# Kernel tuning notes

Hardware: AMD Instinct MI355X
Metric: run time of the kernel (lower is better)

Reference implementation:

```python
import jax, jax.numpy as jnp
import numpy as np

NUM_TEAMS = 200000
EMBED_DIM = 16
NUM_EDGES = 3200000
BATCH = 500000
EPS_NORM = 1e-12  # F.normalize clamp
EPS_SOFTMAX = 1e-16  # PyG edge-softmax denom eps
NEG_SLOPE = 0.01  # LeakyReLU default


def setup_inputs() -> dict:
    key = jax.random.key(0)
    ks = jax.random.split(key, 12)
    inp = {}
    inp["embed"] = jax.random.normal(ks[0], (NUM_TEAMS, EMBED_DIM), dtype=jnp.float32)
    inp["beta"] = jnp.ones((2,), dtype=jnp.float32)  # one learnable scalar per AGNNConv
    # torch Linear init ~ U(-1/sqrt(fan_in), 1/sqrt(fan_in)); stored as [in, out]
    def lin(k, fi, fo):
        b = 1.0 / np.sqrt(fi)
        k1, k2 = jax.random.split(k)
        return (jax.random.uniform(k1, (fi, fo), jnp.float32, -b, b),
                jax.random.uniform(k2, (fo,), jnp.float32, -b, b))
    inp["lin0_w"], inp["lin0_b"] = lin(ks[1], 2 * EMBED_DIM, 6)
    inp["lin1_w"], inp["lin1_b"] = lin(ks[2], 6, 16)
    inp["lin2_w"], inp["lin2_b"] = lin(ks[3], 16, 3)
    inp["edge_index"] = jax.random.randint(ks[4], (2, NUM_EDGES), 0, NUM_TEAMS, dtype=jnp.int64)
    inp["home"] = jax.random.randint(ks[5], (BATCH,), 0, NUM_TEAMS, dtype=jnp.int64)
    inp["away"] = jax.random.randint(ks[6], (BATCH,), 0, NUM_TEAMS, dtype=jnp.int64)
    return inp


def _agnn_conv(x, beta, src, dst, n):
    # x: [N, D]; messages flow src(j) -> dst(i); scatter-softmax over edges per dst
    xn = x / jnp.maximum(jnp.linalg.norm(x, axis=-1, keepdims=True), EPS_NORM)
    alpha = beta * jnp.sum(xn[src] * xn[dst], axis=-1)          # [E]
    m = jax.ops.segment_max(alpha, dst, num_segments=n)          # [N]
    a = jnp.exp(alpha - m[dst])                                   # [E]
    denom = jax.ops.segment_sum(a, dst, num_segments=n)          # [N]
    a = a / (denom[dst] + EPS_SOFTMAX)
    return jax.ops.segment_sum(a[:, None] * x[src], dst, num_segments=n)  # [N, D]


def _forward(embed, beta, lin0_w, lin0_b, lin1_w, lin1_b, lin2_w, lin2_b,
             src, dst, home, away):
    n = embed.shape[0]
    act = lambda v: jax.nn.leaky_relu(v, NEG_SLOPE)
    x = embed  # embedding of arange(n_teams) == the table itself
    x = act(_agnn_conv(x, beta[0], src, dst, n))
    x = act(_agnn_conv(x, beta[1], src, dst, n))
    h = jnp.concatenate([x[home], x[away]], axis=-1)  # [B, 2D]
    h = act(h @ lin0_w + lin0_b)
    h = act(h @ lin1_w + lin1_b)
    h = act(h @ lin2_w + lin2_b)
    return jax.nn.log_softmax(h, axis=0).reshape(-1, 3)  # LogSoftmax(dim=0), faithful


def reference(embed, beta, lin0_w, lin0_b, lin1_w, lin1_b, lin2_w, lin2_b,
              edge_index, home, away):
    n = embed.shape[0]
    # AGNNConv default: remove then add self-loops
    loops = jnp.arange(n, dtype=edge_index.dtype)
    mask = edge_index[0] != edge_index[1]
    safe = jnp.where(mask, edge_index[1], edge_index[0])  # self-loop-out non-loop edges
    src = jnp.concatenate([edge_index[0], loops])
    dst = jnp.concatenate([jnp.where(mask, edge_index[1], edge_index[0]), loops])
    # masked self-loops in original list become src==dst duplicates of the appended
    # self-loops only if random collision; to faithfully *remove* them we redirect
    # removed edges onto the node's own appended self-loop (alpha identical for
    # src==dst), which changes only duplicate self-loop counts with prob ~1/N.
    return _forward(embed, beta, lin0_w, lin0_b, lin1_w, lin1_b, lin2_w, lin2_b,
                    src, dst, home, away)
```

## Files before the change

### kernel.cpp

```cpp
#include <hip/hip_runtime.h>
#include <hip/hip_fp16.h>
#include <math.h>

#define TPB 256
#define NPB 512
#define NPB_SHIFT 9
#define EPB 8192
#define EPW 16
#define BCAP 9216

typedef float v2f __attribute__((ext_vector_type(2)));

__device__ __forceinline__ float leaky_relu(float v) { return v > 0.0f ? v : 0.01f * v; }

__device__ __forceinline__ float dot4(float4 a, float4 b) {
    return a.x * b.x + a.y * b.y + a.z * b.z + a.w * b.w;
}
__device__ __forceinline__ float4 f4_scale(float4 a, float s) {
    return make_float4(a.x * s, a.y * s, a.z * s, a.w * s);
}
__device__ __forceinline__ float4 f4_acc(float4 a, float w, float4 y) {
    return make_float4(fmaf(w, y.x, a.x), fmaf(w, y.y, a.y),
                       fmaf(w, y.z, a.z), fmaf(w, y.w, a.w));
}
__device__ __forceinline__ float4 f4_add_shfl(float4 v, int d) {
    return make_float4(v.x + __shfl_xor(v.x, d, 64), v.y + __shfl_xor(v.y, d, 64),
                       v.z + __shfl_xor(v.z, d, 64), v.w + __shfl_xor(v.w, d, 64));
}
__device__ __forceinline__ float4 leaky4(float4 v) {
    return make_float4(leaky_relu(v.x), leaky_relu(v.y), leaky_relu(v.z), leaky_relu(v.w));
}

__device__ __forceinline__ float4 dec4(unsigned w) {
    v2f lo = __builtin_amdgcn_cvt_pk_f32_fp8((int)w, false);
    v2f hi = __builtin_amdgcn_cvt_pk_f32_fp8((int)w, true);
    return make_float4(lo.x, lo.y, hi.x, hi.y);
}
__device__ __forceinline__ unsigned enc4(float4 v) {
    int r = __builtin_amdgcn_cvt_pk_fp8_f32(v.x, v.y, 0, false);
    r = __builtin_amdgcn_cvt_pk_fp8_f32(v.z, v.w, r, true);
    return (unsigned)r;
}

__device__ __forceinline__ void store_h4(__half* row, int l, float4 v) {
    union { float2 f; __half h[4]; } u;
    u.h[0] = __float2half(v.x); u.h[1] = __float2half(v.y);
    u.h[2] = __float2half(v.z); u.h[3] = __float2half(v.w);
    ((float2*)row)[l] = u.f;
}

__device__ __forceinline__ int wave_incl_scan(int v, int lane) {
#pragma unroll
    for (int off = 1; off < 64; off <<= 1) {
        int u = __shfl_up(v, off, 64);
        if (lane >= off) v += u;
    }
    return v;
}

__global__ void k_binA(const int* __restrict__ src, const int* __restrict__ dst,
                       unsigned* __restrict__ bdata, int* __restrict__ cbase,
                       int* __restrict__ ccnt, int E, int K,
                       const float* __restrict__ x, uint4* __restrict__ xq,
                       int N, int NC) {
    __shared__ int hist[512];
    __shared__ unsigned lcol[EPB];
    __shared__ int wsum[8];
    int t = threadIdx.x;
    int lane = t & 63, wv = t >> 6;
    int c = blockIdx.x;
    int e0 = c * EPB;
    int e1 = min(e0 + EPB, E);
    int tot = e1 - e0;
    hist[t] = 0;
    __syncthreads();
    int myd[EPW], mys[EPW];
    if (tot == EPB) {
        const int4* d4 = (const int4*)(dst + e0);
        const int4* s4 = (const int4*)(src + e0);
#pragma unroll
        for (int k = 0; k < 4; ++k) {
            int4 dd = d4[t + k * 512];
            int4 ss = s4[t + k * 512];
            myd[4 * k + 0] = dd.x; myd[4 * k + 1] = dd.y;
            myd[4 * k + 2] = dd.z; myd[4 * k + 3] = dd.w;
            mys[4 * k + 0] = ss.x; mys[4 * k + 1] = ss.y;
            mys[4 * k + 2] = ss.z; mys[4 * k + 3] = ss.w;
            atomicAdd(&hist[dd.x >> NPB_SHIFT], 1);
            atomicAdd(&hist[dd.y >> NPB_SHIFT], 1);
            atomicAdd(&hist[dd.z >> NPB_SHIFT], 1);
            atomicAdd(&hist[dd.w >> NPB_SHIFT], 1);
        }
    } else {
#pragma unroll
        for (int k = 0; k < EPW; ++k) {
            int e = e0 + t + k * 512;
            int d = (e < e1) ? dst[e] : -1;
            mys[k] = (e < e1) ? src[e] : 0;
            myd[k] = d;
            if (d >= 0) atomicAdd(&hist[d >> NPB_SHIFT], 1);
        }
    }
    __syncthreads();
    int v = hist[t];
    int inc = wave_incl_scan(v, lane);
    if (lane == 63) wsum[wv] = inc;
    __syncthreads();
    if (t == 0) {
        int acc = 0;
#pragma unroll
        for (int k = 0; k < 8; ++k) { int xv = wsum[k]; wsum[k] = acc; acc += xv; }
    }
    __syncthreads();
    int excl = inc + wsum[wv] - v;
    if (t < K) {
        cbase[(size_t)t * NC + c] = excl;
        ccnt[(size_t)t * NC + c] = v;
    }
    __syncthreads();
    hist[t] = excl;
    __syncthreads();
    if (tot == EPB) {
#pragma unroll
        for (int k = 0; k < EPW; ++k) {
            int d = myd[k];
            int p = atomicAdd(&hist[d >> NPB_SHIFT], 1);
            lcol[p] = ((unsigned)(d & (NPB - 1)) << 18) | (unsigned)mys[k];
        }
    } else {
#pragma unroll
        for (int k = 0; k < EPW; ++k) {
            int d = myd[k];
            if (d >= 0) {
                int p = atomicAdd(&hist[d >> NPB_SHIFT], 1);
                lcol[p] = ((unsigned)(d & (NPB - 1)) << 18) | (unsigned)mys[k];
            }
        }
    }
    __syncthreads();
    unsigned* outp = bdata + (size_t)c * EPB;
    for (int i = t; i < tot; i += 512) outp[i] = lcol[i];
    int i = c * 512 + t;
    if (i < N) {
        const float4* xp = (const float4*)(x + (size_t)i * 16);
        float4 a = xp[0], b = xp[1], cc = xp[2], d = xp[3];
        xq[i] = make_uint4(enc4(a), enc4(b), enc4(cc), enc4(d));
    }
}

__global__ void k_binB(const unsigned* __restrict__ bdata, const int* __restrict__ cbase,
                       const int* __restrict__ ccnt,
                       int2* __restrict__ rng, int* __restrict__ col,
                       int N, int NC, int K) {
    __shared__ unsigned raw[BCAP];
    __shared__ int sorted[BCAP];
    __shared__ int ldeg[NPB];
    __shared__ int wsum[8];
    int b = blockIdx.x, t = threadIdx.x;
    int lane = t & 63, wv = t >> 6;
    int n0 = b << NPB_SHIFT;
    int nn = min(NPB, N - n0);
    int mycb = (t < NC) ? cbase[(size_t)b * NC + t] : 0;
    int mycc = (t < NC) ? ccnt[(size_t)b * NC + t] : 0;
    ldeg[t] = 0;
    int inc = wave_incl_scan(mycc, lane);
    if (lane == 63) wsum[wv] = inc;
    __syncthreads();
    if (t == 0) {
        int acc = 0;
#pragma unroll
        for (int k = 0; k < 8; ++k) { int xv = wsum[k]; wsum[k] = acc; acc += xv; }
    }
    __syncthreads();
    int mybase = inc + wsum[wv] - mycc;
    int cnt = wsum[7] + __shfl(inc, 63, 64);
    __syncthreads();
    if (t == 511) wsum[0] = mybase + mycc;
    __syncthreads();
    cnt = wsum[0];
    const unsigned* sp = bdata + (size_t)t * EPB + mycb;
    for (int k = 0; k < mycc; ++k) {
        unsigned tag = sp[k];
        raw[mybase + k] = tag;
        atomicAdd(&ldeg[tag >> 18], 1);
    }
    __syncthreads();
    int dv = ldeg[t];
    int inc2 = wave_incl_scan(dv, lane);
    if (lane == 63) wsum[wv] = inc2;
    __syncthreads();
    if (t == 0) {
        int acc = 0;
#pragma unroll
        for (int k = 0; k < 8; ++k) { int xv = wsum[k]; wsum[k] = acc; acc += xv; }
    }
    __syncthreads();
    int excl = inc2 + wsum[wv] - dv;
    int gb = b * BCAP;
    if (t < nn) rng[n0 + t] = make_int2(gb + excl, gb + excl + dv);
    __syncthreads();
    ldeg[t] = excl;
    __syncthreads();
    for (int i = t; i < cnt; i += 512) {
        unsigned tg = raw[i];
        int pos = atomicAdd(&ldeg[tg >> 18], 1);
        sorted[pos] = (int)(tg & 0x3FFFFu);
    }
    __syncthreads();
    for (int i = t; i < cnt; i += 512) col[gb + i] = sorted[i];
}

__global__ void k_agnn(const uint4* __restrict__ xq,
                       const int2* __restrict__ rng,
                       const int* __restrict__ col,
                       const float* __restrict__ beta_ptr, int beta_idx,
                       void* __restrict__ out, int n, int fp8_out) {
    int t = threadIdx.x;
    int l = t & 7;
    int i = blockIdx.x * (512 / 8) + (t >> 3);
    if (i >= n) return;
    float bet = beta_ptr[beta_idx];
    uint4 rowi = xq[i];
    float4 x0 = dec4(rowi.x), x1 = dec4(rowi.y), x2 = dec4(rowi.z), x3 = dec4(rowi.w);
    float sqi = dot4(x0, x0) + dot4(x1, x1) + dot4(x2, x2) + dot4(x3, x3);
    float inv_ni = rsqrtf(fmaxf(sqi, 1e-24f));
    float bi = bet * inv_ni;
    float4 q0 = f4_scale(x0, bi), q1 = f4_scale(x1, bi),
           q2 = f4_scale(x2, bi), q3 = f4_scale(x3, bi);
    float s;
    float4 a0, a1, a2, a3;
    if (l == 0) {
        float w = __expf(bet);
        s = w;
        a0 = f4_scale(x0, w); a1 = f4_scale(x1, w);
        a2 = f4_scale(x2, w); a3 = f4_scale(x3, w);
    } else {
        s = 0.0f;
        a0 = a1 = a2 = a3 = make_float4(0.f, 0.f, 0.f, 0.f);
    }
    int2 se = rng[i];
    int e1 = se.y;
    int last = max(e1 - 1, 0);
    int e = se.x + l;
    int j0 = min(max(col[min(e, last)], 0), n - 1);
    uint4 rA = xq[j0];
    int j1 = min(max(col[min(e + 8, last)], 0), n - 1);
    uint4 rB = xq[j1];
    for (; e < e1; e += 8) {
        int j2 = min(max(col[min(e + 16, last)], 0), n - 1);
        uint4 rC = xq[j2];
        float4 y0 = dec4(rA.x), y1 = dec4(rA.y), y2 = dec4(rA.z), y3 = dec4(rA.w);
        float sq = dot4(y0, y0) + dot4(y1, y1) + dot4(y2, y2) + dot4(y3, y3);
        float inv_n = rsqrtf(fmaxf(sq, 1e-24f));
        float d = (dot4(y0, q0) + dot4(y1, q1) + dot4(y2, q2) + dot4(y3, q3)) * inv_n;
        float w = __expf(d);
        s += w;
        a0 = f4_acc(a0, w, y0);
        a1 = f4_acc(a1, w, y1);
        a2 = f4_acc(a2, w, y2);
        a3 = f4_acc(a3, w, y3);
        rA = rB; rB = rC;
    }
#pragma unroll
    for (int d_ = 1; d_ < 8; d_ <<= 1) {
        s += __shfl_xor(s, d_, 64);
        a0 = f4_add_shfl(a0, d_);
        a1 = f4_add_shfl(a1, d_);
        a2 = f4_add_shfl(a2, d_);
        a3 = f4_add_shfl(a3, d_);
    }
    float inv = 1.0f / (s + 1e-16f);
    float4 o0 = leaky4(f4_scale(a0, inv));
    float4 o1 = leaky4(f4_scale(a1, inv));
    float4 o2 = leaky4(f4_scale(a2, inv));
    float4 o3 = leaky4(f4_scale(a3, inv));
    if (l < 4) {
        float4 oq = (l == 0) ? o0 : (l == 1) ? o1 : (l == 2) ? o2 : o3;
        if (fp8_out) {
            ((unsigned*)((uint4*)out + i))[l] = enc4(oq);
        } else {
            store_h4((__half*)out + (size_t)i * 16, l, oq);
        }
    }
}

__global__ void k_mlp(const __half* __restrict__ x, const int* __restrict__ home,
                      const int* __restrict__ away,
                      const float* __restrict__ w0, const float* __restrict__ b0,
                      const float* __restrict__ w1, const float* __restrict__ b1,
                      const float* __restrict__ w2, const float* __restrict__ b2,
                      float* __restrict__ z, float* __restrict__ bmax,
                      float* __restrict__ bsum, int nb) {
    __shared__ float sw0[192], sw1[96], sw2[48], sb0[6], sb1[16], sb2[3];
    __shared__ float rmax[4][3];
    __shared__ float rsum[4][3];
    int t = threadIdx.x;
    if (t < 192) sw0[t] = w0[t];
    if (t < 96)  sw1[t] = w1[t];
    if (t < 48)  sw2[t] = w2[t];
    if (t < 6)   sb0[t] = b0[t];
    if (t < 16)  sb1[t] = b1[t];
    if (t < 3)   sb2[t] = b2[t];
    __syncthreads();
    int i = blockIdx.x * blockDim.x + t;
    bool act = i < nb;
    float z0 = -3.4e38f, z1 = -3.4e38f, z2 = -3.4e38f;
    if (act) {
        float h[32];
        const uint4* hr = (const uint4*)(x + (size_t)home[i] * 16);
        const uint4* ar = (const uint4*)(x + (size_t)away[i] * 16);
        uint4 hv0 = hr[0], hv1 = hr[1];
        uint4 av0 = ar[0], av1 = ar[1];
        union { uint4 u; __half2 h2[4]; } cv;
#pragma unroll
        for (int q = 0; q < 4; ++q) {
            cv.u = (q == 0) ? hv0 : (q == 1) ? hv1 : (q == 2) ? av0 : av1;
#pragma unroll
            for (int k = 0; k < 4; ++k) {
                float2 f = __half22float2(cv.h2[k]);
                h[q * 8 + 2 * k + 0] = f.x;
                h[q * 8 + 2 * k + 1] = f.y;
            }
        }
        float t0[6];
#pragma unroll
        for (int o = 0; o < 6; ++o) {
            float acc = sb0[o];
#pragma unroll
            for (int k = 0; k < 32; ++k) acc = fmaf(h[k], sw0[k * 6 + o], acc);
            t0[o] = leaky_relu(acc);
        }
        float t1[16];
#pragma unroll
        for (int o = 0; o < 16; ++o) {
            float acc = sb1[o];
#pragma unroll
            for (int k = 0; k < 6; ++k) acc = fmaf(t0[k], sw1[k * 16 + o], acc);
            t1[o] = leaky_relu(acc);
        }
        float zz[3];
#pragma unroll
        for (int o = 0; o < 3; ++o) {
            float acc = sb2[o];
#pragma unroll
            for (int k = 0; k < 16; ++k) acc = fmaf(t1[k], sw2[k * 3 + o], acc);
            zz[o] = leaky_relu(acc);
            z[(size_t)i * 3 + o] = zz[o];
        }
        z0 = zz[0]; z1 = zz[1]; z2 = zz[2];
    }
    float w0_ = z0, w1_ = z1, w2_ = z2;
#pragma unroll
    for (int off = 32; off > 0; off >>= 1) {
        w0_ = fmaxf(w0_, __shfl_down(w0_, off));
        w1_ = fmaxf(w1_, __shfl_down(w1_, off));
        w2_ = fmaxf(w2_, __shfl_down(w2_, off));
    }
    int wid = t >> 6;
    if ((t & 63) == 0) { rmax[wid][0] = w0_; rmax[wid][1] = w1_; rmax[wid][2] = w2_; }
    __syncthreads();
    float M0 = fmaxf(fmaxf(rmax[0][0], rmax[1][0]), fmaxf(rmax[2][0], rmax[3][0]));
    float M1 = fmaxf(fmaxf(rmax[0][1], rmax[1][1]), fmaxf(rmax[2][1], rmax[3][1]));
    float M2 = fmaxf(fmaxf(rmax[0][2], rmax[1][2]), fmaxf(rmax[2][2], rmax[3][2]));
    float e0 = act ? __expf(z0 - M0) : 0.0f;
    float e1 = act ? __expf(z1 - M1) : 0.0f;
    float e2 = act ? __expf(z2 - M2) : 0.0f;
#pragma unroll
    for (int off = 32; off > 0; off >>= 1) {
        e0 += __shfl_down(e0, off);
        e1 += __shfl_down(e1, off);
        e2 += __shfl_down(e2, off);
    }
    if ((t & 63) == 0) { rsum[wid][0] = e0; rsum[wid][1] = e1; rsum[wid][2] = e2; }
    __syncthreads();
    if (t == 0) {
        float S0 = rsum[0][0] + rsum[1][0] + rsum[2][0] + rsum[3][0];
        float S1 = rsum[0][1] + rsum[1][1] + rsum[2][1] + rsum[3][1];
        float S2 = rsum[0][2] + rsum[1][2] + rsum[2][2] + rsum[3][2];
        bmax[blockIdx.x * 3 + 0] = M0; bmax[blockIdx.x * 3 + 1] = M1; bmax[blockIdx.x * 3 + 2] = M2;
        bsum[blockIdx.x * 3 + 0] = S0; bsum[blockIdx.x * 3 + 1] = S1; bsum[blockIdx.x * 3 + 2] = S2;
    }
}

__device__ __forceinline__ float pick3(int c, float L0, float L1, float L2) {
    return c == 0 ? L0 : (c == 1 ? L1 : L2);
}

__global__ void k_final(const float4* __restrict__ z4,
                        const float* __restrict__ bmax, const float* __restrict__ bsum,
                        int nblk, float4* __restrict__ out4, int n4) {
    __shared__ float lm[4][3];
    __shared__ float ls[4][3];
    __shared__ float Lsh[3];
    int t = threadIdx.x;
    float M0 = -3.4e38f, M1 = -3.4e38f, M2 = -3.4e38f;
    float S0 = 0.f, S1 = 0.f, S2 = 0.f;
    for (int b = t; b < nblk; b += 256) {
        float m0 = bmax[b * 3 + 0], s0 = bsum[b * 3 + 0];
        float n0 = fmaxf(M0, m0); S0 = S0 * __expf(M0 - n0) + s0 * __expf(m0 - n0); M0 = n0;
        float m1 = bmax[b * 3 + 1], s1 = bsum[b * 3 + 1];
        float n1 = fmaxf(M1, m1); S1 = S1 * __expf(M1 - n1) + s1 * __expf(m1 - n1); M1 = n1;
        float m2 = bmax[b * 3 + 2], s2 = bsum[b * 3 + 2];
        float n2 = fmaxf(M2, m2); S2 = S2 * __expf(M2 - n2) + s2 * __expf(m2 - n2); M2 = n2;
    }
#pragma unroll
    for (int off = 32; off > 0; off >>= 1) {
        float mo, so, nm;
        mo = __shfl_down(M0, off); so = __shfl_down(S0, off);
        nm = fmaxf(M0, mo); S0 = S0 * __expf(M0 - nm) + so * __expf(mo - nm); M0 = nm;
        mo = __shfl_down(M1, off); so = __shfl_down(S1, off);
        nm = fmaxf(M1, mo); S1 = S1 * __expf(M1 - nm) + so * __expf(mo - nm); M1 = nm;
        mo = __shfl_down(M2, off); so = __shfl_down(S2, off);
        nm = fmaxf(M2, mo); S2 = S2 * __expf(M2 - nm) + so * __expf(mo - nm); M2 = nm;
    }
    int wid = t >> 6;
    if ((t & 63) == 0) {
        lm[wid][0] = M0; lm[wid][1] = M1; lm[wid][2] = M2;
        ls[wid][0] = S0; ls[wid][1] = S1; ls[wid][2] = S2;
    }
    __syncthreads();
    if (t == 0) {
        for (int w = 1; w < 4; ++w) {
            float nm;
            nm = fmaxf(M0, lm[w][0]); S0 = S0 * __expf(M0 - nm) + ls[w][0] * __expf(lm[w][0] - nm); M0 = nm;
            nm = fmaxf(M1, lm[w][1]); S1 = S1 * __expf(M1 - nm) + ls[w][1] * __expf(lm[w][1] - nm); M1 = nm;
            nm = fmaxf(M2, lm[w][2]); S2 = S2 * __expf(M2 - nm) + ls[w][2] * __expf(lm[w][2] - nm); M2 = nm;
        }
        Lsh[0] = M0 + logf(S0);
        Lsh[1] = M1 + logf(S1);
        Lsh[2] = M2 + logf(S2);
    }
    __syncthreads();
    float L0 = Lsh[0], L1 = Lsh[1], L2 = Lsh[2];
    int i = blockIdx.x * blockDim.x + t;
    if (i >= n4) return;
    float4 v = z4[i];
    int c = i % 3;
    int c1 = (c + 1) % 3, c2 = (c + 2) % 3;
    out4[i] = make_float4(v.x - pick3(c, L0, L1, L2),
                          v.y - pick3(c1, L0, L1, L2),
                          v.z - pick3(c2, L0, L1, L2),
                          v.w - pick3(c, L0, L1, L2));
}

extern "C" void kernel_launch(void* const* d_in, const int* in_sizes, int n_in,
                              void* d_out, int out_size, void* d_ws, size_t ws_size,
                              hipStream_t stream) {
    const float* embed = (const float*)d_in[0];
    const float* beta  = (const float*)d_in[1];
    const float* w0 = (const float*)d_in[2];
    const float* b0 = (const float*)d_in[3];
    const float* w1 = (const float*)d_in[4];
    const float* b1 = (const float*)d_in[5];
    const float* w2 = (const float*)d_in[6];
    const float* b2 = (const float*)d_in[7];
    const int* eidx = (const int*)d_in[8];
    const int* home = (const int*)d_in[9];
    const int* away = (const int*)d_in[10];

    const int N = in_sizes[0] / 16;
    const int E = in_sizes[8] / 2;
    const int B = in_sizes[9];
    const int* esrc = eidx;
    const int* edst = eidx + E;
    const int K = (N + NPB - 1) >> NPB_SHIFT;
    const int NC = (E + EPB - 1) / EPB;

    char* ws = (char*)d_ws;
    size_t off = 0;
    auto alloc = [&](size_t bytes) -> char* {
        off = (off + 255) & ~(size_t)255;
        char* p = ws + off;
        off += bytes;
        return p;
    };
    size_t bdata_bytes = (size_t)NC * EPB * 4;
    size_t alias_bytes = (((size_t)N * 16 + 511) & ~(size_t)255) + (size_t)B * 3 * 4;
    char* U = alloc(bdata_bytes > alias_bytes ? bdata_bytes : alias_bytes);
    unsigned* bdata = (unsigned*)U;
    uint4* xq1  = (uint4*)U;
    float* zbuf = (float*)(U + (((size_t)N * 16 + 511) & ~(size_t)255));

    int2* rng    = (int2*)alloc((size_t)N * 8);
    int* colw    = (int*)alloc((size_t)K * BCAP * 4);
    int* cbase   = (int*)alloc((size_t)K * NC * 4);
    int* ccnt    = (int*)alloc((size_t)K * NC * 4);
    uint4* xq0   = (uint4*)alloc((size_t)N * 16);
    __half* xh2  = (__half*)alloc((size_t)N * 32);
    const int nblkB = (B + TPB - 1) / TPB;
    float* bmax  = (float*)alloc((size_t)nblkB * 3 * 4);
    float* bsum  = (float*)alloc((size_t)nblkB * 3 * 4);
    (void)ws_size; (void)n_in; (void)out_size;

    k_binA<<<NC, 512, 0, stream>>>(esrc, edst, bdata, cbase, ccnt, E, K,
                                   embed, xq0, N, NC);
    k_binB<<<K, 512, 0, stream>>>(bdata, cbase, ccnt, rng, colw, N, NC, K);

    const int nblkN8 = (N + 63) / 64;
    k_agnn<<<nblkN8, 512, 0, stream>>>(xq0, rng, colw, beta, 0, xq1, N, 1);
    k_agnn<<<nblkN8, 512, 0, stream>>>(xq1, rng, colw, beta, 1, xh2, N, 0);

    k_mlp<<<nblkB, TPB, 0, stream>>>(xh2, home, away, w0, b0, w1, b1, w2, b2,
                                     zbuf, bmax, bsum, B);
    const int n4 = (B * 3) / 4;
    k_final<<<(n4 + TPB - 1) / TPB, TPB, 0, stream>>>((const float4*)zbuf, bmax, bsum,
                                                      nblkB, (float4*)d_out, n4);
}
```

Measured before the change: 200.4 us.

## Vectorize bin reads in k_binB and hoist global log-sum-exp into single-block kernel

```diff
diff --git a/kernel.cpp b/kernel.cpp
--- a/kernel.cpp
+++ b/kernel.cpp
@@ -173,16 +173,32 @@
     }
     __syncthreads();
     int mybase = inc + wsum[wv] - mycc;
-    int cnt = wsum[7] + __shfl(inc, 63, 64);
     __syncthreads();
     if (t == 511) wsum[0] = mybase + mycc;
     __syncthreads();
-    cnt = wsum[0];
-    const unsigned* sp = bdata + (size_t)t * EPB + mycb;
-    for (int k = 0; k < mycc; ++k) {
-        unsigned tag = sp[k];
-        raw[mybase + k] = tag;
-        atomicAdd(&ldeg[tag >> 18], 1);
+    int cnt = wsum[0];
+    {
+        const unsigned* sp = bdata + (size_t)t * EPB + mycb;
+        int k = 0;
+        int head = (4 - (mycb & 3)) & 3;
+        if (head > mycc) head = mycc;
+        for (; k < head; ++k) {
+            unsigned tag = sp[k];
+            raw[mybase + k] = tag;
+            atomicAdd(&ldeg[tag >> 18], 1);
+        }
+        for (; k + 4 <= mycc; k += 4) {
+            uint4 vq = *(const uint4*)(sp + k);
+            raw[mybase + k + 0] = vq.x; atomicAdd(&ldeg[vq.x >> 18], 1);
+            raw[mybase + k + 1] = vq.y; atomicAdd(&ldeg[vq.y >> 18], 1);
+            raw[mybase + k + 2] = vq.z; atomicAdd(&ldeg[vq.z >> 18], 1);
+            raw[mybase + k + 3] = vq.w; atomicAdd(&ldeg[vq.w >> 18], 1);
+        }
+        for (; k < mycc; ++k) {
+            unsigned tag = sp[k];
+            raw[mybase + k] = tag;
+            atomicAdd(&ldeg[tag >> 18], 1);
+        }
     }
     __syncthreads();
     int dv = ldeg[t];
@@ -382,16 +398,10 @@
     }
 }
 
-__device__ __forceinline__ float pick3(int c, float L0, float L1, float L2) {
-    return c == 0 ? L0 : (c == 1 ? L1 : L2);
-}
-
-__global__ void k_final(const float4* __restrict__ z4,
-                        const float* __restrict__ bmax, const float* __restrict__ bsum,
-                        int nblk, float4* __restrict__ out4, int n4) {
+__global__ void k_lse(const float* __restrict__ bmax, const float* __restrict__ bsum,
+                      float* __restrict__ gL, int nblk) {
     __shared__ float lm[4][3];
     __shared__ float ls[4][3];
-    __shared__ float Lsh[3];
     int t = threadIdx.x;
     float M0 = -3.4e38f, M1 = -3.4e38f, M2 = -3.4e38f;
     float S0 = 0.f, S1 = 0.f, S2 = 0.f;
@@ -426,14 +436,21 @@
             nm = fmaxf(M1, lm[w][1]); S1 = S1 * __expf(M1 - nm) + ls[w][1] * __expf(lm[w][1] - nm); M1 = nm;
             nm = fmaxf(M2, lm[w][2]); S2 = S2 * __expf(M2 - nm) + ls[w][2] * __expf(lm[w][2] - nm); M2 = nm;
         }
-        Lsh[0] = M0 + logf(S0);
-        Lsh[1] = M1 + logf(S1);
-        Lsh[2] = M2 + logf(S2);
-    }
-    __syncthreads();
-    float L0 = Lsh[0], L1 = Lsh[1], L2 = Lsh[2];
-    int i = blockIdx.x * blockDim.x + t;
+        gL[0] = M0 + logf(S0);
+        gL[1] = M1 + logf(S1);
+        gL[2] = M2 + logf(S2);
+    }
+}
+
+__device__ __forceinline__ float pick3(int c, float L0, float L1, float L2) {
+    return c == 0 ? L0 : (c == 1 ? L1 : L2);
+}
+
+__global__ void k_final(const float4* __restrict__ z4, const float* __restrict__ gL,
+                        float4* __restrict__ out4, int n4) {
+    int i = blockIdx.x * blockDim.x + threadIdx.x;
     if (i >= n4) return;
+    float L0 = gL[0], L1 = gL[1], L2 = gL[2];
     float4 v = z4[i];
     int c = i % 3;
     int c1 = (c + 1) % 3, c2 = (c + 2) % 3;
@@ -490,6 +507,7 @@
     const int nblkB = (B + TPB - 1) / TPB;
     float* bmax  = (float*)alloc((size_t)nblkB * 3 * 4);
     float* bsum  = (float*)alloc((size_t)nblkB * 3 * 4);
+    float* gL    = (float*)alloc(16);
     (void)ws_size; (void)n_in; (void)out_size;
 
     k_binA<<<NC, 512, 0, stream>>>(esrc, edst, bdata, cbase, ccnt, E, K,
@@ -502,7 +520,8 @@
 
     k_mlp<<<nblkB, TPB, 0, stream>>>(xh2, home, away, w0, b0, w1, b1, w2, b2,
                                      zbuf, bmax, bsum, B);
+    k_lse<<<1, 256, 0, stream>>>(bmax, bsum, gL, nblkB);
     const int n4 = (B * 3) / 4;
-    k_final<<<(n4 + TPB - 1) / TPB, TPB, 0, stream>>>((const float4*)zbuf, bmax, bsum,
-                                                      nblkB, (float4*)d_out, n4);
-}
+    k_final<<<(n4 + TPB - 1) / TPB, TPB, 0, stream>>>((const float4*)zbuf, gL,
+                                                      (float4*)d_out, n4);
+}
```

Measured after the change: 198.1 us. No clear change (-1.2%).
